# Kernel optimization log

Measured on AMD Instinct MI355X. Metric: run time of the kernel, lower is better.

The kernel has to match this reference:

```python
import jax, jax.numpy as jnp
import numpy as np

N = 100000      # nodes
E = 1600000     # edges (avg degree 16)
F_IN = 256      # Data.num_features
H = 128         # hidden_channels
C = 10          # num classes


def setup_inputs() -> dict:
    key = jax.random.key(0)
    ks = jax.random.split(key, 5)
    x = jax.random.normal(ks[0], (N, F_IN), dtype=jnp.float32)
    edge_index = jax.random.randint(ks[1], (2, E), 0, N, dtype=jnp.int32)
    W1 = jax.random.normal(ks[2], (F_IN, H), dtype=jnp.float32) / np.sqrt(F_IN)
    b1 = jnp.zeros((H,), dtype=jnp.float32)
    W2 = jax.random.normal(ks[3], (H, C), dtype=jnp.float32) / np.sqrt(H)
    b2 = jnp.zeros((C,), dtype=jnp.float32)
    return {"x": x, "edge_index": edge_index, "W1": W1, "b1": b1, "W2": W2, "b2": b2}


def _gcn_conv(x, W, b, src, dst, dinv_sqrt):
    # dense transform first (PyG GCNConv order), then normalized gather-scatter
    h = x @ W                                   # [N, out]
    norm = dinv_sqrt[src] * dinv_sqrt[dst]      # [E+N]
    msg = h[src] * norm[:, None]                # [E+N, out]
    out = jax.ops.segment_sum(msg, dst, num_segments=N)
    return out + b


def reference(x, edge_index, W1, b1, W2, b2):
    # add self-loops (GCNConv default)
    loop = jnp.arange(N, dtype=edge_index.dtype)
    src = jnp.concatenate([edge_index[0], loop])
    dst = jnp.concatenate([edge_index[1], loop])
    # symmetric normalization: D^-1/2 (A+I) D^-1/2, degree counted on dst
    deg = jax.ops.segment_sum(jnp.ones_like(dst, dtype=x.dtype), dst, num_segments=N)
    dinv_sqrt = jnp.where(deg > 0, jax.lax.rsqrt(deg), 0.0)
    h = _gcn_conv(x, W1, b1, src, dst, dinv_sqrt)
    h = jax.nn.relu(h)
    h = _gcn_conv(h, W2, b2, src, dst, dinv_sqrt)
    return jax.nn.log_softmax(h, axis=1)
```

## Files before the change

### kernel.cpp

```cpp
#include <hip/hip_runtime.h>
#include <math.h>

#define BLK 256
#define BKT_BITS 9
#define BKT (1<<BKT_BITS)
#define MAXNB 256
#define EB 8192
#define BSTRIDE 16384

typedef __attribute__((ext_vector_type(8))) short bf16x8;
typedef __attribute__((ext_vector_type(4))) float f32x4;

__device__ inline unsigned short f2b(float f){
  union { float f; unsigned int u; } v; v.f = f;
  unsigned int u = v.u;
  return (unsigned short)((u + 0x7FFF + ((u >> 16) & 1)) >> 16);
}
__device__ inline float b2f_lo(unsigned int u){
  union { unsigned int u; float f; } v; v.u = u << 16; return v.f;
}
__device__ inline float b2f_hi(unsigned int u){
  union { unsigned int u; float f; } v; v.u = u & 0xFFFF0000u; return v.f;
}
__device__ inline unsigned pkbf(float lo, float hi){
  unsigned r;
  asm("v_cvt_pk_bf16_f32 %0, %1, %2" : "=v"(r) : "v"(lo), "v"(hi));
  return r;
}


__global__ __launch_bounds__(256)
void binC(const int* __restrict__ src, const int* __restrict__ dst,
          int* __restrict__ bcnt, unsigned int* __restrict__ bins, int E, int NB){
  __shared__ int lh[MAXNB];
  __shared__ int lofs[MAXNB];
  __shared__ int lcur[MAXNB];
  __shared__ int gres[MAXNB];
  __shared__ int sscan[256];
  __shared__ __attribute__((aligned(16))) int2 buf[EB];
  int t = threadIdx.x;
  for (int i=t;i<MAXNB;i+=256) lh[i]=0;
  __syncthreads();
  int base = blockIdx.x*EB;
  #pragma unroll
  for (int k=0;k<EB/1024;k++){
    int idx = base + (k*256 + t)*4;
    if (idx < E){
      int4 d = *(const int4*)(dst + idx);
      atomicAdd(&lh[d.x>>BKT_BITS],1);
      atomicAdd(&lh[d.y>>BKT_BITS],1);
      atomicAdd(&lh[d.z>>BKT_BITS],1);
      atomicAdd(&lh[d.w>>BKT_BITS],1);
    }
  }
  __syncthreads();
  int v0 = lh[t];
  sscan[t] = v0; __syncthreads();
  for (int off=1; off<256; off<<=1){
    int v = (t>=off)? sscan[t-off]:0;
    __syncthreads();
    sscan[t]+=v;
    __syncthreads();
  }
  lofs[t] = sscan[t]-v0;
  lcur[t] = sscan[t]-v0;
  if (t < NB)
    gres[t] = lh[t] ? (t*BSTRIDE + atomicAdd(&bcnt[t], lh[t])) : 0;
  __syncthreads();
  #pragma unroll
  for (int k=0;k<EB/1024;k++){
    int idx = base + (k*256 + t)*4;
    if (idx < E){
      int4 s4 = *(const int4*)(src + idx);
      int4 d4 = *(const int4*)(dst + idx);
      int p;
      p = atomicAdd(&lcur[d4.x>>BKT_BITS],1); buf[p] = make_int2(s4.x,d4.x);
      p = atomicAdd(&lcur[d4.y>>BKT_BITS],1); buf[p] = make_int2(s4.y,d4.y);
      p = atomicAdd(&lcur[d4.z>>BKT_BITS],1); buf[p] = make_int2(s4.z,d4.z);
      p = atomicAdd(&lcur[d4.w>>BKT_BITS],1); buf[p] = make_int2(s4.w,d4.w);
    }
  }
  __syncthreads();
  int total = E - base; if (total > EB) total = EB;
  for (int i=t; i<total; i+=256){
    int2 pr = buf[i];
    int b = pr.y>>BKT_BITS;
    bins[gres[b] + (i - lofs[b])] = ((unsigned)pr.x << BKT_BITS) | (unsigned)(pr.y & (BKT-1));
  }
}

__global__ __launch_bounds__(256)
void bfill_all(const unsigned int* __restrict__ bins, const int* __restrict__ bcnt,
               int* __restrict__ rowptr, float* __restrict__ dinv, int* __restrict__ col,
               const float* __restrict__ W1, unsigned short* __restrict__ W1T,
               int N, int NB){
  int b = blockIdx.x;
  if (b >= NB){
    int t2 = (b - NB)*256 + threadIdx.x;
    if (t2 < 256*128){
      int k = t2 >> 7, n = t2 & 127;
      W1T[n*256 + k] = f2b(W1[t2]);
    }
    return;
  }
  __shared__ int dcnt[BKT];
  __shared__ int rp[BKT];
  __shared__ int cur[BKT];
  __shared__ int sscan[256];
  __shared__ int sboff;
  int t = threadIdx.x;
  int partial = 0;
  for (int j=t; j<b; j+=256) partial += bcnt[j];
  if (t==0) sboff = 0;
  dcnt[t] = 0; dcnt[t+256] = 0;
  __syncthreads();
  if (partial) atomicAdd(&sboff, partial);
  __syncthreads();
  int s = sboff, cnt = bcnt[b];
  const unsigned int* mybins = bins + (size_t)b*BSTRIDE;
  for (int i=t;i<cnt;i+=256) atomicAdd(&dcnt[mybins[i] & (BKT-1)], 1);
  __syncthreads();
  int base = b<<BKT_BITS;
  int i0 = 2*t, i1 = 2*t+1;
  int d0 = dcnt[i0], d1 = dcnt[i1];
  int n0 = (base+i0 < N) ? d0+1 : 0;
  int n1 = (base+i1 < N) ? d1+1 : 0;
  int tsum = n0+n1;
  sscan[t] = tsum; __syncthreads();
  for (int off=1; off<256; off<<=1){
    int v = (t>=off)? sscan[t-off]:0;
    __syncthreads();
    sscan[t]+=v;
    __syncthreads();
  }
  int run = sscan[t]-tsum;
  int gstart = s + base;
  int rp0 = gstart + run, rp1 = rp0 + n0;
  rp[i0] = rp0; rp[i1] = rp1;
  cur[i0] = 0;  cur[i1] = 0;
  if (base+i0 < N){
    rowptr[base+i0] = rp0;
    dinv[base+i0] = rsqrtf((float)(d0+1));
    if (base+i0 == N-1) rowptr[N] = rp0 + d0 + 1;
  }
  if (base+i1 < N){
    rowptr[base+i1] = rp1;
    dinv[base+i1] = rsqrtf((float)(d1+1));
    if (base+i1 == N-1) rowptr[N] = rp1 + d1 + 1;
  }
  __syncthreads();
  for (int i=t;i<cnt;i+=256){
    unsigned pk = mybins[i];
    int ln = pk & (BKT-1);
    int slot = atomicAdd(&cur[ln], 1);
    col[rp[ln] + slot] = (int)(pk >> BKT_BITS);
  }
  __syncthreads();
  for (int i=t;i<BKT;i+=256){
    int node = base+i;
    if (node < N) col[rp[i] + dcnt[i]] = node;
  }
}


__global__ __launch_bounds__(512)
void gemm1_mfma(const float* __restrict__ X, const unsigned short* __restrict__ W1T,
                const float* __restrict__ dinv, unsigned short* __restrict__ H1B, int M){
  __shared__ __attribute__((aligned(16))) unsigned short wsh[64*512];
  const int tid = threadIdx.x;
  const int wave = tid >> 6, lane = tid & 63;
  const int quad = lane >> 4, l16 = lane & 15;

  #pragma unroll
  for (int f0=0; f0<64; f0+=8){
    int f = f0 + wave;
    int ct = f >> 3, ts = f & 7;
    uint4 v = *(const uint4*)(W1T + (ct*16 + l16)*256 + ts*32 + quad*8);
    *(uint4*)(wsh + f*512 + lane*8) = v;
  }
  __syncthreads();

  const int row0 = blockIdx.x * 256 + wave * 32;
  int rA = row0 + l16;
  int rB = rA + 16;
  int rAc = (rA < M) ? rA : (M-1);
  int rBc = (rB < M) ? rB : (M-1);
  const float* xA = X + (size_t)rAc*256 + quad*8;
  const float* xB = X + (size_t)rBc*256 + quad*8;

  f32x4 acc[2][8];
  #pragma unroll
  for (int i=0;i<2;i++)
    #pragma unroll
    for (int j=0;j<8;j++) acc[i][j] = (f32x4){0.f,0.f,0.f,0.f};

  float4 pf[2][4];
  #pragma unroll
  for (int s=0;s<2;s++){
    pf[s][0] = *(const float4*)(xA + s*32);
    pf[s][1] = *(const float4*)(xA + s*32 + 4);
    pf[s][2] = *(const float4*)(xB + s*32);
    pf[s][3] = *(const float4*)(xB + s*32 + 4);
  }

  #pragma unroll
  for (int t=0; t<8; t++){
    const int cur = t & 1;
    union { bf16x8 v; unsigned u[4]; } fa, fb;
    fa.u[0] = pkbf(pf[cur][0].x, pf[cur][0].y);
    fa.u[1] = pkbf(pf[cur][0].z, pf[cur][0].w);
    fa.u[2] = pkbf(pf[cur][1].x, pf[cur][1].y);
    fa.u[3] = pkbf(pf[cur][1].z, pf[cur][1].w);
    fb.u[0] = pkbf(pf[cur][2].x, pf[cur][2].y);
    fb.u[1] = pkbf(pf[cur][2].z, pf[cur][2].w);
    fb.u[2] = pkbf(pf[cur][3].x, pf[cur][3].y);
    fb.u[3] = pkbf(pf[cur][3].z, pf[cur][3].w);
    if (t < 6){
      pf[cur][0] = *(const float4*)(xA + (t+2)*32);
      pf[cur][1] = *(const float4*)(xA + (t+2)*32 + 4);
      pf[cur][2] = *(const float4*)(xB + (t+2)*32);
      pf[cur][3] = *(const float4*)(xB + (t+2)*32 + 4);
    }
    #pragma unroll
    for (int ct=0; ct<8; ct++){
      bf16x8 bf = *(const bf16x8*)(wsh + (ct*8 + t)*512 + lane*8);
      acc[0][ct] = __builtin_amdgcn_mfma_f32_16x16x32_bf16(fa.v, bf, acc[0][ct], 0, 0, 0);
      acc[1][ct] = __builtin_amdgcn_mfma_f32_16x16x32_bf16(fb.v, bf, acc[1][ct], 0, 0, 0);
    }
  }

  #pragma unroll
  for (int rt=0; rt<2; rt++){
    int rbase = row0 + rt*16 + quad*4;
    #pragma unroll
    for (int rg=0; rg<4; rg++){
      int grow = rbase + rg;
      if (grow < M){
        float dv = dinv[grow];
        #pragma unroll
        for (int ct=0; ct<8; ct++)
          H1B[(size_t)grow*128 + ct*16 + l16] = f2b(dv * acc[rt][ct][rg]);
      }
    }
  }
}


__device__ inline void acc8(float* a, uint4 u){
  a[0]+=b2f_lo(u.x); a[1]+=b2f_hi(u.x); a[2]+=b2f_lo(u.y); a[3]+=b2f_hi(u.y);
  a[4]+=b2f_lo(u.z); a[5]+=b2f_hi(u.z); a[6]+=b2f_lo(u.w); a[7]+=b2f_hi(u.w);
}

__global__ __launch_bounds__(256)
void agg1_kernel(const unsigned short* __restrict__ H1B, const int* __restrict__ rowptr,
                 const int* __restrict__ col, const float* __restrict__ dinv,
                 const float* __restrict__ b1, unsigned int* __restrict__ R1B, int N){
  int node = blockIdx.x * 4 + (threadIdx.x >> 6);
  int lane = threadIdx.x & 63;
  int g   = lane >> 4;
  int l16 = lane & 15;
  if (node >= N) return;
  int s = rowptr[node], e = rowptr[node+1];
  float a[8];
  #pragma unroll
  for (int k=0;k<8;k++) a[k]=0.f;
  const char* hbase = (const char*)H1B + l16*16;
  int j = s;
  for (; j+15 < e; j+=16){
    int c0 = col[j+g], c1 = col[j+4+g], c2 = col[j+8+g], c3 = col[j+12+g];
    uint4 u0 = *(const uint4*)(hbase + (((unsigned)c0) << 8));
    uint4 u1 = *(const uint4*)(hbase + (((unsigned)c1) << 8));
    uint4 u2 = *(const uint4*)(hbase + (((unsigned)c2) << 8));
    uint4 u3 = *(const uint4*)(hbase + (((unsigned)c3) << 8));
    acc8(a, u0); acc8(a, u1); acc8(a, u2); acc8(a, u3);
  }
  for (; j+7 < e; j+=8){
    int c0 = col[j+g], c1 = col[j+4+g];
    uint4 u0 = *(const uint4*)(hbase + (((unsigned)c0) << 8));
    uint4 u1 = *(const uint4*)(hbase + (((unsigned)c1) << 8));
    acc8(a, u0); acc8(a, u1);
  }
  {
    int rem = e - j;
    if (g < rem){
      int c0 = col[j+g];
      uint4 u0 = *(const uint4*)(hbase + (((unsigned)c0) << 8));
      acc8(a, u0);
    }
    if (g+4 < rem){
      int c1 = col[j+4+g];
      uint4 u1 = *(const uint4*)(hbase + (((unsigned)c1) << 8));
      acc8(a, u1);
    }
  }
  #pragma unroll
  for (int k=0;k<8;k++){
    a[k] += __shfl_xor(a[k], 16);
    a[k] += __shfl_xor(a[k], 32);
  }
  if (g == 0){
    float dv = dinv[node];
    float4 bl = *(const float4*)(b1 + l16*8);
    float4 bh = *(const float4*)(b1 + l16*8 + 4);
    float f0, f1;
    unsigned int o0, o1, o2, o3;
    f0 = fmaxf(dv*a[0] + bl.x, 0.f); f1 = fmaxf(dv*a[1] + bl.y, 0.f);
    o0 = (unsigned)f2b(f0) | ((unsigned)f2b(f1) << 16);
    f0 = fmaxf(dv*a[2] + bl.z, 0.f); f1 = fmaxf(dv*a[3] + bl.w, 0.f);
    o1 = (unsigned)f2b(f0) | ((unsigned)f2b(f1) << 16);
    f0 = fmaxf(dv*a[4] + bh.x, 0.f); f1 = fmaxf(dv*a[5] + bh.y, 0.f);
    o2 = (unsigned)f2b(f0) | ((unsigned)f2b(f1) << 16);
    f0 = fmaxf(dv*a[6] + bh.z, 0.f); f1 = fmaxf(dv*a[7] + bh.w, 0.f);
    o3 = (unsigned)f2b(f0) | ((unsigned)f2b(f1) << 16);
    *(uint4*)(R1B + (size_t)node*64 + l16*4) = make_uint4(o0, o1, o2, o3);
  }
}


__global__ __launch_bounds__(256)
void gemm2_kernel(const unsigned int* __restrict__ R1B, const float* __restrict__ W2,
                  const float* __restrict__ dinv, unsigned int* __restrict__ H2B, int M){
  __shared__ float w2s[128*10];
  for (int i = threadIdx.x; i < 128*10; i += blockDim.x) w2s[i] = W2[i];
  __syncthreads();
  int r = blockIdx.x*blockDim.x + threadIdx.x;
  if (r >= M) return;
  float acc[10];
  #pragma unroll
  for (int c=0;c<10;c++) acc[c] = 0.f;
  const unsigned int* row = R1B + (size_t)r*64;
  for (int k=0;k<64;k+=4){
    uint4 u = *(const uint4*)(row + k);
    float f0 = b2f_lo(u.x), f1 = b2f_hi(u.x);
    float f2 = b2f_lo(u.y), f3 = b2f_hi(u.y);
    float f4 = b2f_lo(u.z), f5 = b2f_hi(u.z);
    float f6 = b2f_lo(u.w), f7 = b2f_hi(u.w);
    #pragma unroll
    for (int c=0;c<10;c++){
      acc[c] += f0*w2s[(2*k+0)*10+c] + f1*w2s[(2*k+1)*10+c]
              + f2*w2s[(2*k+2)*10+c] + f3*w2s[(2*k+3)*10+c]
              + f4*w2s[(2*k+4)*10+c] + f5*w2s[(2*k+5)*10+c]
              + f6*w2s[(2*k+6)*10+c] + f7*w2s[(2*k+7)*10+c];
    }
  }
  float dv = dinv[r];
  unsigned int p[5];
  #pragma unroll
  for (int c=0;c<5;c++)
    p[c] = (unsigned)f2b(dv*acc[2*c]) | ((unsigned)f2b(dv*acc[2*c+1]) << 16);
  unsigned int* op = H2B + (size_t)r*8;
  *(uint4*)op = make_uint4(p[0],p[1],p[2],p[3]);
  *(uint4*)(op+4) = make_uint4(p[4],0u,0u,0u);
}


__global__ __launch_bounds__(256)
void agg2_softmax_kernel(const unsigned int* __restrict__ H2B, const int* __restrict__ rowptr,
                         const int* __restrict__ col, const float* __restrict__ dinv,
                         const float* __restrict__ b2, float* __restrict__ out, int N){
  int tid = threadIdx.x;
  int node = blockIdx.x * 16 + (tid >> 4);
  int l16 = tid & 15;
  int g2 = l16 >> 3;
  int l8 = l16 & 7;
  if (node >= N) return;
  int s = rowptr[node], e = rowptr[node+1];
  float aLo = 0.f, aHi = 0.f, bLo = 0.f, bHi = 0.f;
  const unsigned int* hb = H2B + l8;
  int j = s;
  for (; j+3 < e; j += 4){
    unsigned u0 = hb[(size_t)col[j+g2]*8];
    unsigned u1 = hb[(size_t)col[j+2+g2]*8];
    aLo += b2f_lo(u0); aHi += b2f_hi(u0);
    bLo += b2f_lo(u1); bHi += b2f_hi(u1);
  }
  for (; j+1 < e; j += 2){
    unsigned u0 = hb[(size_t)col[j+g2]*8];
    aLo += b2f_lo(u0); aHi += b2f_hi(u0);
  }
  if (j < e && g2 == 0){
    unsigned u0 = hb[(size_t)col[j]*8];
    aLo += b2f_lo(u0); aHi += b2f_hi(u0);
  }
  aLo += bLo; aHi += bHi;
  aLo += __shfl_xor(aLo, 8);
  aHi += __shfl_xor(aHi, 8);
  float dv = dinv[node];
  float2 bb = (l8 < 5) ? *(const float2*)(b2 + 2*l8) : make_float2(0.f, 0.f);
  float c0 = (l8 < 5) ? (dv*aLo + bb.x) : -1e30f;
  float c1 = (l8 < 5) ? (dv*aHi + bb.y) : -1e30f;
  float m = fmaxf(c0, c1);
  m = fmaxf(m, __shfl_xor(m, 1));
  m = fmaxf(m, __shfl_xor(m, 2));
  m = fmaxf(m, __shfl_xor(m, 4));
  float ex = (l8 < 5) ? (expf(c0 - m) + expf(c1 - m)) : 0.f;
  ex += __shfl_xor(ex, 1);
  ex += __shfl_xor(ex, 2);
  ex += __shfl_xor(ex, 4);
  float lg = m + logf(ex);
  if (l8 < 5 && g2 == 0)
    *(float2*)(out + (size_t)node*10 + 2*l8) = make_float2(c0 - lg, c1 - lg);
}


extern "C" void kernel_launch(void* const* d_in, const int* in_sizes, int n_in,
                              void* d_out, int out_size, void* d_ws, size_t ws_size,
                              hipStream_t stream){
  const float* x    = (const float*)d_in[0];
  const int*   ei   = (const int*)d_in[1];
  const float* W1   = (const float*)d_in[2];
  const float* b1   = (const float*)d_in[3];
  const float* W2   = (const float*)d_in[4];
  const float* b2   = (const float*)d_in[5];
  float* out = (float*)d_out;

  const int N = in_sizes[0] / 256;
  const int E = in_sizes[1] / 2;
  const int NNZ = E + N;
  const int* src = ei;
  const int* dst = ei + E;
  const int NB = (N + BKT - 1) >> BKT_BITS;
  const int WB = 128;

  char* ws = (char*)d_ws;
  size_t off = 0;
  auto alloc = [&](size_t bytes)->char*{
    char* p = ws + off;
    off = (off + bytes + 255) & ~(size_t)255;
    return p;
  };
  int*   bcnt   = (int*)  alloc((size_t)MAXNB*4);
  float* dinv   = (float*)alloc((size_t)N*4);
  int*   rowptr = (int*)  alloc((size_t)(N+1)*4);
  unsigned int* bins = (unsigned int*)alloc((size_t)NB*BSTRIDE*4);
  int*   col    = (int*)  alloc((size_t)NNZ*4);
  unsigned short* w1t = (unsigned short*)alloc((size_t)128*256*2);
  unsigned short* h1b = (unsigned short*)alloc((size_t)N*128*2);
  unsigned int*   r1b = (unsigned int*)  alloc((size_t)N*64*4);
  unsigned int*   h2b = (unsigned int*)  alloc((size_t)N*8*4);
  (void)ws_size;

  hipMemsetAsync(bcnt, 0, (size_t)MAXNB*4, stream);

  const int NCB = (E + EB - 1) / EB;

  binC<<<NCB, 256, 0, stream>>>(src, dst, bcnt, bins, E, NB);
  bfill_all<<<NB + WB, 256, 0, stream>>>(bins, bcnt, rowptr, dinv, col, W1, w1t, N, NB);

  gemm1_mfma<<<(N+255)/256, 512, 0, stream>>>(x, w1t, dinv, h1b, N);
  agg1_kernel<<<(N+3)/4, 256, 0, stream>>>(h1b, rowptr, col, dinv, b1, r1b, N);
  gemm2_kernel<<<(N+BLK-1)/BLK, BLK, 0, stream>>>(r1b, W2, dinv, h2b, N);
  agg2_softmax_kernel<<<(N+15)/16, BLK, 0, stream>>>(h2b, rowptr, col, dinv, b2, out, N);
}
```

Measured before the change: 319.3 us.

## Replace bucketed CSR build with global atomic degree count, scan, and fill

Replaces the two-pass bucket-binning CSR construction (shared-memory bucket sort into a staging bins array, then a per-bucket fill) with three simpler kernels. A global-atomic degree histogram is computed, a per-block prefix scan produces rowptr, dinv and the self-loop entries, and a final pass scatters source indices using global atomic cursors. This drops the large intermediate bins buffer and its write and read traffic. In exchange it adds many scattered global atomics, one more kernel launch, and a scan whose per-block prefix sum rereads the whole preceding degree array. Neighbour order within each row now depends on atomic timing.

```diff
diff --git a/kernel.cpp b/kernel.cpp
--- a/kernel.cpp
+++ b/kernel.cpp
@@ -4,9 +4,6 @@
 #define BLK 256
 #define BKT_BITS 9
 #define BKT (1<<BKT_BITS)
-#define MAXNB 256
-#define EB 8192
-#define BSTRIDE 16384
 
 typedef __attribute__((ext_vector_type(8))) short bf16x8;
 typedef __attribute__((ext_vector_type(4))) float f32x4;
@@ -30,101 +27,48 @@
 
 
 __global__ __launch_bounds__(256)
-void binC(const int* __restrict__ src, const int* __restrict__ dst,
-          int* __restrict__ bcnt, unsigned int* __restrict__ bins, int E, int NB){
-  __shared__ int lh[MAXNB];
-  __shared__ int lofs[MAXNB];
-  __shared__ int lcur[MAXNB];
-  __shared__ int gres[MAXNB];
-  __shared__ int sscan[256];
-  __shared__ __attribute__((aligned(16))) int2 buf[EB];
-  int t = threadIdx.x;
-  for (int i=t;i<MAXNB;i+=256) lh[i]=0;
-  __syncthreads();
-  int base = blockIdx.x*EB;
-  #pragma unroll
-  for (int k=0;k<EB/1024;k++){
-    int idx = base + (k*256 + t)*4;
-    if (idx < E){
-      int4 d = *(const int4*)(dst + idx);
-      atomicAdd(&lh[d.x>>BKT_BITS],1);
-      atomicAdd(&lh[d.y>>BKT_BITS],1);
-      atomicAdd(&lh[d.z>>BKT_BITS],1);
-      atomicAdd(&lh[d.w>>BKT_BITS],1);
-    }
-  }
-  __syncthreads();
-  int v0 = lh[t];
-  sscan[t] = v0; __syncthreads();
-  for (int off=1; off<256; off<<=1){
-    int v = (t>=off)? sscan[t-off]:0;
-    __syncthreads();
-    sscan[t]+=v;
-    __syncthreads();
-  }
-  lofs[t] = sscan[t]-v0;
-  lcur[t] = sscan[t]-v0;
-  if (t < NB)
-    gres[t] = lh[t] ? (t*BSTRIDE + atomicAdd(&bcnt[t], lh[t])) : 0;
-  __syncthreads();
-  #pragma unroll
-  for (int k=0;k<EB/1024;k++){
-    int idx = base + (k*256 + t)*4;
-    if (idx < E){
-      int4 s4 = *(const int4*)(src + idx);
-      int4 d4 = *(const int4*)(dst + idx);
-      int p;
-      p = atomicAdd(&lcur[d4.x>>BKT_BITS],1); buf[p] = make_int2(s4.x,d4.x);
-      p = atomicAdd(&lcur[d4.y>>BKT_BITS],1); buf[p] = make_int2(s4.y,d4.y);
-      p = atomicAdd(&lcur[d4.z>>BKT_BITS],1); buf[p] = make_int2(s4.z,d4.z);
-      p = atomicAdd(&lcur[d4.w>>BKT_BITS],1); buf[p] = make_int2(s4.w,d4.w);
-    }
-  }
-  __syncthreads();
-  int total = E - base; if (total > EB) total = EB;
-  for (int i=t; i<total; i+=256){
-    int2 pr = buf[i];
-    int b = pr.y>>BKT_BITS;
-    bins[gres[b] + (i - lofs[b])] = ((unsigned)pr.x << BKT_BITS) | (unsigned)(pr.y & (BKT-1));
-  }
-}
-
-__global__ __launch_bounds__(256)
-void bfill_all(const unsigned int* __restrict__ bins, const int* __restrict__ bcnt,
-               int* __restrict__ rowptr, float* __restrict__ dinv, int* __restrict__ col,
-               const float* __restrict__ W1, unsigned short* __restrict__ W1T,
-               int N, int NB){
+void deg_w1t(const int* __restrict__ dst, int* __restrict__ deg,
+             const float* __restrict__ W1, unsigned short* __restrict__ W1T,
+             int E, int NQB){
   int b = blockIdx.x;
-  if (b >= NB){
-    int t2 = (b - NB)*256 + threadIdx.x;
+  if (b >= NQB){
+    int t2 = (b - NQB)*256 + threadIdx.x;
     if (t2 < 256*128){
       int k = t2 >> 7, n = t2 & 127;
       W1T[n*256 + k] = f2b(W1[t2]);
     }
     return;
   }
-  __shared__ int dcnt[BKT];
-  __shared__ int rp[BKT];
-  __shared__ int cur[BKT];
+  int idx = (b*256 + threadIdx.x)*4;
+  if (idx < E){
+    int4 d = *(const int4*)(dst + idx);
+    atomicAdd(&deg[d.x],1);
+    atomicAdd(&deg[d.y],1);
+    atomicAdd(&deg[d.z],1);
+    atomicAdd(&deg[d.w],1);
+  }
+}
+
+__global__ __launch_bounds__(256)
+void scan_k(const int* __restrict__ deg, int* __restrict__ rowptr,
+            int* __restrict__ wcur, float* __restrict__ dinv,
+            int* __restrict__ col, int N){
   __shared__ int sscan[256];
   __shared__ int sboff;
+  int b = blockIdx.x;
   int t = threadIdx.x;
+  if (t==0) sboff = 0;
+  __syncthreads();
+  int base = b << BKT_BITS;
   int partial = 0;
-  for (int j=t; j<b; j+=256) partial += bcnt[j];
-  if (t==0) sboff = 0;
-  dcnt[t] = 0; dcnt[t+256] = 0;
-  __syncthreads();
+  for (int j=t; j<base; j+=256) partial += deg[j];
   if (partial) atomicAdd(&sboff, partial);
   __syncthreads();
-  int s = sboff, cnt = bcnt[b];
-  const unsigned int* mybins = bins + (size_t)b*BSTRIDE;
-  for (int i=t;i<cnt;i+=256) atomicAdd(&dcnt[mybins[i] & (BKT-1)], 1);
-  __syncthreads();
-  int base = b<<BKT_BITS;
-  int i0 = 2*t, i1 = 2*t+1;
-  int d0 = dcnt[i0], d1 = dcnt[i1];
-  int n0 = (base+i0 < N) ? d0+1 : 0;
-  int n1 = (base+i1 < N) ? d1+1 : 0;
+  int i0 = base + 2*t, i1 = base + 2*t + 1;
+  int d0 = (i0 < N) ? deg[i0] : 0;
+  int d1 = (i1 < N) ? deg[i1] : 0;
+  int n0 = (i0 < N) ? d0+1 : 0;
+  int n1 = (i1 < N) ? d1+1 : 0;
   int tsum = n0+n1;
   sscan[t] = tsum; __syncthreads();
   for (int off=1; off<256; off<<=1){
@@ -134,31 +78,34 @@
     __syncthreads();
   }
   int run = sscan[t]-tsum;
-  int gstart = s + base;
-  int rp0 = gstart + run, rp1 = rp0 + n0;
-  rp[i0] = rp0; rp[i1] = rp1;
-  cur[i0] = 0;  cur[i1] = 0;
-  if (base+i0 < N){
-    rowptr[base+i0] = rp0;
-    dinv[base+i0] = rsqrtf((float)(d0+1));
-    if (base+i0 == N-1) rowptr[N] = rp0 + d0 + 1;
-  }
-  if (base+i1 < N){
-    rowptr[base+i1] = rp1;
-    dinv[base+i1] = rsqrtf((float)(d1+1));
-    if (base+i1 == N-1) rowptr[N] = rp1 + d1 + 1;
-  }
-  __syncthreads();
-  for (int i=t;i<cnt;i+=256){
-    unsigned pk = mybins[i];
-    int ln = pk & (BKT-1);
-    int slot = atomicAdd(&cur[ln], 1);
-    col[rp[ln] + slot] = (int)(pk >> BKT_BITS);
-  }
-  __syncthreads();
-  for (int i=t;i<BKT;i+=256){
-    int node = base+i;
-    if (node < N) col[rp[i] + dcnt[i]] = node;
+  int gbase = sboff + base;
+  int rp0 = gbase + run, rp1 = rp0 + n0;
+  if (i0 < N){
+    rowptr[i0] = rp0; wcur[i0] = rp0;
+    dinv[i0] = rsqrtf((float)(d0+1));
+    col[rp0 + d0] = i0;
+    if (i0 == N-1) rowptr[N] = rp0 + d0 + 1;
+  }
+  if (i1 < N){
+    rowptr[i1] = rp1; wcur[i1] = rp1;
+    dinv[i1] = rsqrtf((float)(d1+1));
+    col[rp1 + d1] = i1;
+    if (i1 == N-1) rowptr[N] = rp1 + d1 + 1;
+  }
+}
+
+__global__ __launch_bounds__(256)
+void fill_k(const int* __restrict__ src, const int* __restrict__ dst,
+            int* __restrict__ wcur, int* __restrict__ col, int E){
+  int idx = (blockIdx.x*256 + threadIdx.x)*4;
+  if (idx < E){
+    int4 s4 = *(const int4*)(src + idx);
+    int4 d4 = *(const int4*)(dst + idx);
+    int p0 = atomicAdd(&wcur[d4.x],1);
+    int p1 = atomicAdd(&wcur[d4.y],1);
+    int p2 = atomicAdd(&wcur[d4.z],1);
+    int p3 = atomicAdd(&wcur[d4.w],1);
+    col[p0] = s4.x; col[p1] = s4.y; col[p2] = s4.z; col[p3] = s4.w;
   }
 }
 
@@ -429,10 +376,10 @@
     off = (off + bytes + 255) & ~(size_t)255;
     return p;
   };
-  int*   bcnt   = (int*)  alloc((size_t)MAXNB*4);
+  int*   deg    = (int*)  alloc((size_t)N*4);
+  int*   wcur   = (int*)  alloc((size_t)N*4);
   float* dinv   = (float*)alloc((size_t)N*4);
   int*   rowptr = (int*)  alloc((size_t)(N+1)*4);
-  unsigned int* bins = (unsigned int*)alloc((size_t)NB*BSTRIDE*4);
   int*   col    = (int*)  alloc((size_t)NNZ*4);
   unsigned short* w1t = (unsigned short*)alloc((size_t)128*256*2);
   unsigned short* h1b = (unsigned short*)alloc((size_t)N*128*2);
@@ -440,12 +387,13 @@
   unsigned int*   h2b = (unsigned int*)  alloc((size_t)N*8*4);
   (void)ws_size;
 
-  hipMemsetAsync(bcnt, 0, (size_t)MAXNB*4, stream);
-
-  const int NCB = (E + EB - 1) / EB;
-
-  binC<<<NCB, 256, 0, stream>>>(src, dst, bcnt, bins, E, NB);
-  bfill_all<<<NB + WB, 256, 0, stream>>>(bins, bcnt, rowptr, dinv, col, W1, w1t, N, NB);
+  hipMemsetAsync(deg, 0, (size_t)N*4, stream);
+
+  const int NQB = (E/4 + 255) / 256;
+
+  deg_w1t<<<NQB + WB, 256, 0, stream>>>(dst, deg, W1, w1t, E, NQB);
+  scan_k<<<NB, 256, 0, stream>>>(deg, rowptr, wcur, dinv, col, N);
+  fill_k<<<NQB, 256, 0, stream>>>(src, dst, wcur, col, E);
 
   gemm1_mfma<<<(N+255)/256, 512, 0, stream>>>(x, w1t, dinv, h1b, N);
   agg1_kernel<<<(N+3)/4, 256, 0, stream>>>(h1b, rowptr, col, dinv, b1, r1b, N);
```

After: 519.4 us. 62.7% more time.
